# Optimization experiments

Measured on AMD Instinct MI355X. Metric: run time of the kernel, lower is better.

Reference implementation:

```python
import jax, jax.numpy as jnp
import numpy as np
import math

N_HIDDEN = 256
N_BLOCKS = 15
N_BINARY = 8
NODE_DIM = 16
EDGE_DIM = 4
N_NODES = 20000
N_EDGES = 100000


def setup_inputs() -> dict:
    key = jax.random.key(0)
    ks = iter(jax.random.split(key, 64))

    def lin(i, o):
        return (jax.random.normal(next(ks), (i, o), jnp.float32) / np.sqrt(i)).astype(jnp.float32)

    def lin_s(i, o):  # stacked over N_BLOCKS layers
        return (jax.random.normal(next(ks), (N_BLOCKS, i, o), jnp.float32) / np.sqrt(i)).astype(jnp.float32)

    inp = {
        "x": jax.random.uniform(next(ks), (N_NODES, NODE_DIM), jnp.float32),
        "edge_index": jax.random.randint(next(ks), (2, N_EDGES), 0, N_NODES, jnp.int32),
        "edge_attr": jax.random.uniform(next(ks), (N_EDGES, EDGE_DIM), jnp.float32),
        # conv1: in = NODE_DIM
        "Wq1": lin(NODE_DIM, N_HIDDEN), "bq1": jnp.zeros((N_HIDDEN,), jnp.float32),
        "Wk1": lin(NODE_DIM, N_HIDDEN), "bk1": jnp.zeros((N_HIDDEN,), jnp.float32),
        "Wv1": lin(NODE_DIM, N_HIDDEN), "bv1": jnp.zeros((N_HIDDEN,), jnp.float32),
        "We1": lin(EDGE_DIM, N_HIDDEN),  # lin_edge has no bias in PyG TransformerConv
        "Ws1": lin(NODE_DIM, N_HIDDEN), "bs1": jnp.zeros((N_HIDDEN,), jnp.float32),
        # 15 residual blocks: in = N_HIDDEN, stacked params
        "Wq": lin_s(N_HIDDEN, N_HIDDEN), "bq": jnp.zeros((N_BLOCKS, N_HIDDEN), jnp.float32),
        "Wk": lin_s(N_HIDDEN, N_HIDDEN), "bk": jnp.zeros((N_BLOCKS, N_HIDDEN), jnp.float32),
        "Wv": lin_s(N_HIDDEN, N_HIDDEN), "bv": jnp.zeros((N_BLOCKS, N_HIDDEN), jnp.float32),
        "We": lin_s(EDGE_DIM, N_HIDDEN),
        "Ws": lin_s(N_HIDDEN, N_HIDDEN), "bs": jnp.zeros((N_BLOCKS, N_HIDDEN), jnp.float32),
        # output head
        "Wl": lin(N_HIDDEN, N_BINARY), "bl": jnp.zeros((N_BINARY,), jnp.float32),
        "scale": jnp.asarray([2.0 ** i for i in range(N_BINARY)], jnp.float32),
    }
    return inp


def _tconv(h, ea_emb_src_params, src, dst, n):
    """PyG TransformerConv (heads=1) with edge features."""
    wq, bq, wk, bk, wv, bv, we, ws, bs, ea = ea_emb_src_params
    q = h @ wq + bq          # [N, C]
    k = h @ wk + bk
    v = h @ wv + bv
    e = ea @ we              # [E, C] edge embedding
    ke = k[src] + e          # [E, C]
    alpha = jnp.sum(q[dst] * ke, axis=-1) / math.sqrt(N_HIDDEN)  # [E]
    m = jax.ops.segment_max(alpha, dst, num_segments=n)
    a = jnp.exp(alpha - m[dst])
    s = jax.ops.segment_sum(a, dst, num_segments=n)
    attn = a / (s[dst] + 1e-16)
    out = jax.ops.segment_sum(attn[:, None] * (v[src] + e), dst, num_segments=n)
    return out + h @ ws + bs  # root_weight skip


def reference(x, edge_index, edge_attr,
              Wq1, bq1, Wk1, bk1, Wv1, bv1, We1, Ws1, bs1,
              Wq, bq, Wk, bk, Wv, bv, We, Ws, bs,
              Wl, bl, scale):
    n = x.shape[0]
    src, dst = edge_index[0], edge_index[1]
    h = jnp.log(x + 1.0)
    ea = jnp.log(edge_attr + 1.0)
    h = _tconv(h, (Wq1, bq1, Wk1, bk1, Wv1, bv1, We1, Ws1, bs1, ea), src, dst, n)

    def block(carry, p):
        wq, bq_, wk, bk_, wv, bv_, we, ws, bs_ = p
        std = jax.lax.stop_gradient(jnp.std(carry, axis=-1, ddof=1, keepdims=True))
        h2 = jax.nn.relu(carry / std)
        y = _tconv(h2, (wq, bq_, wk, bk_, wv, bv_, we, ws, bs_, ea), src, dst, n)
        return carry + y, None

    h, _ = jax.lax.scan(block, h, (Wq, bq, Wk, bk, Wv, bv, We, Ws, bs))
    h = h / math.sqrt(N_BLOCKS)
    h = h @ Wl + bl
    return jnp.sum(h * scale, axis=-1, keepdims=True)
```

## Files before the change

### kernel.cpp

```cpp
#include <hip/hip_runtime.h>
#include <math.h>

typedef short bf16x8 __attribute__((ext_vector_type(8)));
typedef float f32x4 __attribute__((ext_vector_type(4)));
typedef _Float16 h16x8 __attribute__((ext_vector_type(8)));
typedef _Float16 h16x4 __attribute__((ext_vector_type(4)));
typedef _Float16 h16x2 __attribute__((ext_vector_type(2)));

static __device__ __forceinline__ float wred_sum(float v){
  #pragma unroll
  for (int o = 32; o > 0; o >>= 1) v += __shfl_xor(v, o, 64);
  return v;
}

static __device__ __forceinline__ unsigned short f2bf(float x){
  union { float f; unsigned int u; } c; c.f = x;
  unsigned int u = c.u;
  return (unsigned short)((u + 0x7FFFu + ((u >> 16) & 1u)) >> 16);
}

__global__ void prep_kernel(const float* __restrict__ x, const float* __restrict__ ea_in,
                            float* __restrict__ hx, float* __restrict__ ea,
                            int nx, int ne){
  int i = blockIdx.x * 256 + threadIdx.x;
  if (i < nx) hx[i] = logf(x[i] + 1.f);
  if (i < ne) ea[i] = logf(ea_in[i] + 1.f);
}

__global__ void zero_kernel(int* __restrict__ c, int n){
  int i = blockIdx.x * 256 + threadIdx.x;
  if (i < n) c[i] = 0;
}

__global__ void hist_kernel(const int* __restrict__ dst, int* __restrict__ counts, int E){
  int i = blockIdx.x * 256 + threadIdx.x;
  if (i < E) atomicAdd(&counts[dst[i]], 1);
}

__global__ __launch_bounds__(1024) void scan_kernel(const int* __restrict__ counts,
                                                    int* __restrict__ row_ptr,
                                                    int* __restrict__ cursor, int N){
  __shared__ int sh[1024];
  __shared__ int carry_s;
  int t = threadIdx.x;
  if (t == 0) carry_s = 0;
  __syncthreads();
  for (int base = 0; base < N; base += 1024){
    int i = base + t;
    int v = (i < N) ? counts[i] : 0;
    sh[t] = v;
    __syncthreads();
    for (int o = 1; o < 1024; o <<= 1){
      int add = (t >= o) ? sh[t - o] : 0;
      __syncthreads();
      sh[t] += add;
      __syncthreads();
    }
    int incl = sh[t];
    int carry = carry_s;
    if (i < N){ int ex = carry + incl - v; row_ptr[i] = ex; cursor[i] = ex; }
    __syncthreads();
    if (t == 1023) carry_s = carry + incl;
    __syncthreads();
  }
  if (t == 0) row_ptr[N] = carry_s;
}

__global__ void scatter_kernel(const int* __restrict__ src, const int* __restrict__ dst,
                               const float* __restrict__ ea,
                               int* __restrict__ cursor,
                               int* __restrict__ src_csr, float* __restrict__ ea_csr, int E){
  int i = blockIdx.x * 256 + threadIdx.x;
  if (i < E){
    int p = atomicAdd(&cursor[dst[i]], 1);
    src_csr[p] = src[i];
    *(float4*)&ea_csr[(size_t)p * 4] = *(const float4*)&ea[(size_t)i * 4];
  }
}

__global__ void wlscale_kernel(const float* __restrict__ Wl, const float* __restrict__ bl,
                               const float* __restrict__ scale, float* __restrict__ wlsc){
  int c = threadIdx.x;
  float s = 0.f;
  #pragma unroll
  for (int j = 0; j < 8; j++) s += Wl[c * 8 + j] * scale[j];
  wlsc[c] = s;
  if (c == 0){
    float b = 0.f;
    #pragma unroll
    for (int j = 0; j < 8; j++) b += bl[j] * scale[j];
    wlsc[256] = b;
  }
}

__global__ __launch_bounds__(256) void pack_w_kernel(
    const float* __restrict__ Wq, const float* __restrict__ Wk,
    const float* __restrict__ Wv, const float* __restrict__ Ws,
    unsigned short* __restrict__ Wp)
{
  __shared__ float t[32][33];
  int l   = blockIdx.z;
  int k0  = blockIdx.x * 32;
  int n0g = blockIdx.y * 32;
  int w   = n0g >> 8;
  int n0  = n0g & 255;
  const float* W = ((w == 0) ? Wq : (w == 1) ? Wk : (w == 2) ? Wv : Ws) + (size_t)l * 65536;
  int rr = threadIdx.x >> 3;
  int cc = (threadIdx.x & 7) * 4;
  float4 vv = *(const float4*)&W[(size_t)(k0 + rr) * 256 + n0 + cc];
  t[rr][cc + 0] = vv.x; t[rr][cc + 1] = vv.y; t[rr][cc + 2] = vv.z; t[rr][cc + 3] = vv.w;
  __syncthreads();
  ushort4 o;
  o.x = f2bf(t[cc + 0][rr]);
  o.y = f2bf(t[cc + 1][rr]);
  o.z = f2bf(t[cc + 2][rr]);
  o.w = f2bf(t[cc + 3][rr]);
  *(ushort4*)&Wp[(size_t)l * 262144 + (size_t)(n0g + rr) * 256 + k0 + cc] = o;
}

__global__ void pack_b_kernel(const float* __restrict__ bq, const float* __restrict__ bk,
                              const float* __restrict__ bv, const float* __restrict__ bs,
                              float* __restrict__ bp){
  int i = blockIdx.x * 256 + threadIdx.x;
  if (i < 15 * 256){
    int l = i >> 8, n = i & 255;
    bp[l * 1024 + 0   + n] = bq[i];
    bp[l * 1024 + 256 + n] = bk[i];
    bp[l * 1024 + 512 + n] = bv[i];
    bp[l * 1024 + 768 + n] = bs[i];
  }
}

__global__ __launch_bounds__(256) void pack_wqe_kernel(
    const float* __restrict__ Wq, const float* __restrict__ We,
    const float* __restrict__ bq, float* __restrict__ Wqe, float* __restrict__ bqe)
{
  __shared__ float We_s[1024];
  int l = blockIdx.x;
  for (int i = threadIdx.x; i < 1024; i += 256) We_s[i] = We[(size_t)l * 1024 + i];
  __syncthreads();
  int k = threadIdx.x;
  const float* wrow = Wq + (size_t)l * 65536 + (size_t)k * 256;
  float s0 = 0.f, s1 = 0.f, s2 = 0.f, s3 = 0.f;
  for (int c = 0; c < 256; c++){
    float wv = wrow[c];
    s0 += wv * We_s[c];
    s1 += wv * We_s[256 + c];
    s2 += wv * We_s[512 + c];
    s3 += wv * We_s[768 + c];
  }
  float4 o; o.x = s0; o.y = s1; o.z = s2; o.w = s3;
  *(float4*)&Wqe[((size_t)l * 256 + k) * 4] = o;
  if (k < 4){
    float b = 0.f;
    for (int c = 0; c < 256; c++) b += bq[l * 256 + c] * We_s[k * 256 + c];
    bqe[l * 4 + k] = b;
  }
}

__global__ __launch_bounds__(256) void qwe1_kernel(const _Float16* __restrict__ qkvh,
                                                   const float* __restrict__ We1,
                                                   float* __restrict__ qwe, int N){
  __shared__ float We_s[1024];
  for (int i = threadIdx.x; i < 1024; i += 256) We_s[i] = We1[i];
  __syncthreads();
  int wid = threadIdx.x >> 6, lane = threadIdx.x & 63;
  int n = blockIdx.x * 4 + wid;
  if (n >= N) return;
  int c0 = lane * 4;
  h16x4 qr = *(const h16x4*)&qkvh[(size_t)n * 768 + c0];
  float q0 = (float)qr[0], q1 = (float)qr[1], q2 = (float)qr[2], q3 = (float)qr[3];
  float4 o;
  #pragma unroll
  for (int j = 0; j < 4; j++){
    float s = q0 * We_s[j * 256 + c0] + q1 * We_s[j * 256 + c0 + 1]
            + q2 * We_s[j * 256 + c0 + 2] + q3 * We_s[j * 256 + c0 + 3];
    s = wred_sum(s);
    if (j == 0) o.x = s; else if (j == 1) o.y = s; else if (j == 2) o.z = s; else o.w = s;
  }
  if (lane == 0) *(float4*)&qwe[(size_t)n * 4] = o;
}

__global__ __launch_bounds__(256) void gemm1_kernel(
    const float* __restrict__ A,
    const float* __restrict__ W0, const float* __restrict__ W1,
    const float* __restrict__ W2, const float* __restrict__ W3,
    const float* __restrict__ B0, const float* __restrict__ B1,
    const float* __restrict__ B2, const float* __restrict__ B3,
    _Float16* __restrict__ qkvh, _Float16* __restrict__ slh, int N)
{
  __shared__ float As[64][16];
  int nb = blockIdx.x * 64;
  {
    int row = nb + (threadIdx.x >> 2);
    int qq = (threadIdx.x & 3) * 4;
    float4 a = make_float4(0.f, 0.f, 0.f, 0.f);
    if (row < N) a = *(const float4*)&A[row * 16 + qq];
    *(float4*)&As[threadIdx.x >> 2][qq] = a;
  }
  __syncthreads();
  int col = threadIdx.x;
  #pragma unroll
  for (int w = 0; w < 4; w++){
    const float* W  = (w == 0) ? W0 : (w == 1) ? W1 : (w == 2) ? W2 : W3;
    const float* Bi = (w == 0) ? B0 : (w == 1) ? B1 : (w == 2) ? B2 : B3;
    float wr[16];
    #pragma unroll
    for (int kk = 0; kk < 16; kk++) wr[kk] = W[kk * 256 + col];
    float bias = Bi[col];
    for (int r = 0; r < 64; r++){
      int row = nb + r;
      if (row >= N) break;
      float acc = bias;
      #pragma unroll
      for (int kk = 0; kk < 16; kk++) acc += As[r][kk] * wr[kk];
      if (w < 3) qkvh[(size_t)row * 768 + w * 256 + col] = (_Float16)acc;
      else       slh[(size_t)row * 256 + col] = (_Float16)acc;
    }
  }
}

__global__ __launch_bounds__(256, 2) void gemm_mfma_kernel(
    const unsigned short* __restrict__ A,
    const unsigned short* __restrict__ Wp,
    const float* __restrict__ bp,
    _Float16* __restrict__ qkvh,
    _Float16* __restrict__ slh,
    int M)
{
  __shared__ unsigned short lds[2 * 128 * 64];
  unsigned short* ldsA = lds;
  unsigned short* ldsB = lds + 128 * 64;
  const int tid  = threadIdx.x;
  const int wave = tid >> 6, lane = tid & 63;
  const int wm = wave >> 1, wn = wave & 1;
  const int m0 = blockIdx.x * 128;
  const int n0 = blockIdx.y * 128;

  f32x4 acc[4][4] = {};

  const int srow  = lane >> 3;
  const int sc16  = lane & 7;
  const int skgrp = sc16 ^ (srow & 7);

  for (int k0 = 0; k0 < 256; k0 += 64){
    #pragma unroll
    for (int it = 0; it < 4; ++it){
      int lrow = wave * 32 + it * 8;
      const unsigned short* gA = A + (size_t)(m0 + lrow + srow) * 256 + k0 + skgrp * 8;
      __builtin_amdgcn_global_load_lds((const __attribute__((address_space(1))) unsigned int*)gA,
          (__attribute__((address_space(3))) unsigned int*)(ldsA + lrow * 64), 16, 0, 0);
      const unsigned short* gB = Wp + (size_t)(n0 + lrow + srow) * 256 + k0 + skgrp * 8;
      __builtin_amdgcn_global_load_lds((const __attribute__((address_space(1))) unsigned int*)gB,
          (__attribute__((address_space(3))) unsigned int*)(ldsB + lrow * 64), 16, 0, 0);
    }
    __syncthreads();

    bf16x8 af[4][2], bfr[4][2];
    #pragma unroll
    for (int mb = 0; mb < 4; ++mb){
      int r = wm * 64 + mb * 16 + (lane & 15);
      #pragma unroll
      for (int ks = 0; ks < 2; ++ks){
        int kg = ks * 4 + (lane >> 4);
        af[mb][ks] = *(const bf16x8*)&ldsA[r * 64 + ((kg ^ (r & 7)) * 8)];
      }
    }
    #pragma unroll
    for (int nb = 0; nb < 4; ++nb){
      int r = wn * 64 + nb * 16 + (lane & 15);
      #pragma unroll
      for (int ks = 0; ks < 2; ++ks){
        int kg = ks * 4 + (lane >> 4);
        bfr[nb][ks] = *(const bf16x8*)&ldsB[r * 64 + ((kg ^ (r & 7)) * 8)];
      }
    }
    #pragma unroll
    for (int mb = 0; mb < 4; ++mb){
      #pragma unroll
      for (int nb = 0; nb < 4; ++nb){
        acc[mb][nb] = __builtin_amdgcn_mfma_f32_16x16x32_bf16(af[mb][0], bfr[nb][0], acc[mb][nb], 0, 0, 0);
        acc[mb][nb] = __builtin_amdgcn_mfma_f32_16x16x32_bf16(af[mb][1], bfr[nb][1], acc[mb][nb], 0, 0, 0);
      }
    }
    __syncthreads();
  }

  #pragma unroll
  for (int nb = 0; nb < 4; ++nb){
    int col = n0 + wn * 64 + nb * 16 + (lane & 15);
    float bias = bp[col];
    #pragma unroll
    for (int mb = 0; mb < 4; ++mb){
      #pragma unroll
      for (int r4 = 0; r4 < 4; ++r4){
        int row = m0 + wm * 64 + mb * 16 + (lane >> 4) * 4 + r4;
        if (row < M){
          float o = acc[mb][nb][r4] + bias;
          if (col < 768) qkvh[(size_t)row * 768 + col] = (_Float16)o;
          else           slh[(size_t)row * 256 + (col - 768)] = (_Float16)o;
        }
      }
    }
  }
}

__global__ __launch_bounds__(256) void agg_kernel(
    const _Float16* __restrict__ qkvh,
    const _Float16* __restrict__ slh,
    const float* __restrict__ qwe,
    const float* __restrict__ ea_csr,
    const int* __restrict__ src_csr,
    const float* __restrict__ We,
    const float* __restrict__ Wqe_next,
    const float* __restrict__ bqe_next,
    const int* __restrict__ row_ptr,
    const float* __restrict__ h_in, float* __restrict__ h_out,
    unsigned short* __restrict__ h2b, float* __restrict__ qwe_out,
    int RESID, int N)
{
  int wid = threadIdx.x >> 6, lane = threadIdx.x & 63;
  int n = blockIdx.x * 4 + wid;
  if (n >= N) return;
  int c0 = lane * 4;
  int glane = lane >> 4;
  int slane = lane & 15;

  float4 qwe4 = *(const float4*)&qwe[(size_t)n * 4];
  const _Float16* qrow = qkvh + (size_t)n * 768 + slane * 16;
  union { h16x8 v; h16x2 p[4]; } qa, qb;
  qa.v = *(const h16x8*)qrow;
  qb.v = *(const h16x8*)(qrow + 8);

  float m = -INFINITY, ssum = 0.f;
  float a0 = 0.f, a1 = 0.f, a2 = 0.f, a3 = 0.f;
  float ec0 = 0.f, ec1 = 0.f, ec2 = 0.f, ec3 = 0.f;
  int e0 = row_ptr[n], e1 = row_ptr[n + 1];

  for (int base = e0; base < e1; base += 4){
    int cnt = min(4, e1 - base);
    int eg = base + ((glane < cnt) ? glane : (cnt - 1));
    int sg = src_csr[eg];
    float4 eag = *(const float4*)&ea_csr[(size_t)eg * 4];
    const _Float16* krow = qkvh + (size_t)sg * 768 + 256 + slane * 16;
    union { h16x8 v; h16x2 p[4]; } ka, kb;
    ka.v = *(const h16x8*)krow;
    kb.v = *(const h16x8*)(krow + 8);
    float dot = 0.f;
    #pragma unroll
    for (int u = 0; u < 4; ++u){
#if __has_builtin(__builtin_amdgcn_fdot2)
      dot = __builtin_amdgcn_fdot2(qa.p[u], ka.p[u], dot, false);
      dot = __builtin_amdgcn_fdot2(qb.p[u], kb.p[u], dot, false);
#else
      dot += (float)qa.p[u][0] * (float)ka.p[u][0] + (float)qa.p[u][1] * (float)ka.p[u][1];
      dot += (float)qb.p[u][0] * (float)kb.p[u][0] + (float)qb.p[u][1] * (float)kb.p[u][1];
#endif
    }
    #pragma unroll
    for (int o = 1; o < 16; o <<= 1) dot += __shfl_xor(dot, o, 64);
    float alpha_g = (dot + qwe4.x * eag.x + qwe4.y * eag.y + qwe4.z * eag.z + qwe4.w * eag.w) * 0.0625f;
    float aj[4];
    #pragma unroll
    for (int j = 0; j < 4; ++j){
      aj[j] = __shfl(alpha_g, j << 4, 64);
      if (j >= cnt) aj[j] = -INFINITY;
    }
    float mc = fmaxf(fmaxf(aj[0], aj[1]), fmaxf(aj[2], aj[3]));
    float mn = fmaxf(m, mc);
    float corr = expf(m - mn);
    float w0 = (0 < cnt) ? expf(aj[0] - mn) : 0.f;
    float w1 = (1 < cnt) ? expf(aj[1] - mn) : 0.f;
    float w2 = (2 < cnt) ? expf(aj[2] - mn) : 0.f;
    float w3 = (3 < cnt) ? expf(aj[3] - mn) : 0.f;
    ssum = ssum * corr + (w0 + w1 + w2 + w3);
    a0 *= corr; a1 *= corr; a2 *= corr; a3 *= corr;
    ec0 *= corr; ec1 *= corr; ec2 *= corr; ec3 *= corr;
    m = mn;
    float wj[4] = {w0, w1, w2, w3};
    #pragma unroll
    for (int j = 0; j < 4; ++j){
      if (j < cnt){
        int sj = __shfl(sg, j << 4, 64);
        h16x4 vr = *(const h16x4*)&qkvh[(size_t)sj * 768 + 512 + c0];
        float4 er = *(const float4*)&ea_csr[(size_t)(base + j) * 4];
        a0 += wj[j] * (float)vr[0];
        a1 += wj[j] * (float)vr[1];
        a2 += wj[j] * (float)vr[2];
        a3 += wj[j] * (float)vr[3];
        ec0 += wj[j] * er.x;
        ec1 += wj[j] * er.y;
        ec2 += wj[j] * er.z;
        ec3 += wj[j] * er.w;
      }
    }
  }

  float inv = 1.f / (ssum + 1e-16f);
  float4 W0 = *(const float4*)&We[0 * 256 + c0];
  float4 W1 = *(const float4*)&We[1 * 256 + c0];
  float4 W2 = *(const float4*)&We[2 * 256 + c0];
  float4 W3 = *(const float4*)&We[3 * 256 + c0];
  float emb0 = ec0 * W0.x + ec1 * W1.x + ec2 * W2.x + ec3 * W3.x;
  float emb1 = ec0 * W0.y + ec1 * W1.y + ec2 * W2.y + ec3 * W3.y;
  float emb2 = ec0 * W0.z + ec1 * W1.z + ec2 * W2.z + ec3 * W3.z;
  float emb3 = ec0 * W0.w + ec1 * W1.w + ec2 * W2.w + ec3 * W3.w;
  h16x4 slv4 = *(const h16x4*)&slh[(size_t)n * 256 + c0];
  float y0 = (a0 + emb0) * inv + (float)slv4[0];
  float y1 = (a1 + emb1) * inv + (float)slv4[1];
  float y2 = (a2 + emb2) * inv + (float)slv4[2];
  float y3 = (a3 + emb3) * inv + (float)slv4[3];
  float o0, o1, o2, o3;
  if (RESID){
    float4 hp = *(const float4*)&h_in[(size_t)n * 256 + c0];
    o0 = hp.x + y0; o1 = hp.y + y1; o2 = hp.z + y2; o3 = hp.w + y3;
  } else {
    o0 = y0; o1 = y1; o2 = y2; o3 = y3;
  }
  float4 ho; ho.x = o0; ho.y = o1; ho.z = o2; ho.w = o3;
  *(float4*)&h_out[(size_t)n * 256 + c0] = ho;
  float mean = wred_sum(o0 + o1 + o2 + o3) * (1.f / 256.f);
  float d0 = o0 - mean, d1 = o1 - mean, d2 = o2 - mean, d3 = o3 - mean;
  float var = wred_sum(d0 * d0 + d1 * d1 + d2 * d2 + d3 * d3) * (1.f / 255.f);
  float invstd = 1.f / sqrtf(var);
  float t0 = fmaxf(o0 * invstd, 0.f);
  float t1 = fmaxf(o1 * invstd, 0.f);
  float t2 = fmaxf(o2 * invstd, 0.f);
  float t3 = fmaxf(o3 * invstd, 0.f);
  ushort4 hb;
  hb.x = f2bf(t0); hb.y = f2bf(t1); hb.z = f2bf(t2); hb.w = f2bf(t3);
  *(ushort4*)&h2b[(size_t)n * 256 + c0] = hb;
  if (Wqe_next){
    float4 g0 = *(const float4*)&Wqe_next[(c0 + 0) * 4];
    float4 g1 = *(const float4*)&Wqe_next[(c0 + 1) * 4];
    float4 g2 = *(const float4*)&Wqe_next[(c0 + 2) * 4];
    float4 g3 = *(const float4*)&Wqe_next[(c0 + 3) * 4];
    float s0 = t0 * g0.x + t1 * g1.x + t2 * g2.x + t3 * g3.x;
    float s1 = t0 * g0.y + t1 * g1.y + t2 * g2.y + t3 * g3.y;
    float s2 = t0 * g0.z + t1 * g1.z + t2 * g2.z + t3 * g3.z;
    float s3 = t0 * g0.w + t1 * g1.w + t2 * g2.w + t3 * g3.w;
    s0 = wred_sum(s0); s1 = wred_sum(s1); s2 = wred_sum(s2); s3 = wred_sum(s3);
    if (lane == 0){
      float4 bq4 = *(const float4*)bqe_next;
      float4 o; o.x = s0 + bq4.x; o.y = s1 + bq4.y; o.z = s2 + bq4.z; o.w = s3 + bq4.w;
      *(float4*)&qwe_out[(size_t)n * 4] = o;
    }
  }
}

__global__ __launch_bounds__(256) void head_kernel(const float* __restrict__ h,
                                                   const float* __restrict__ wlsc,
                                                   float* __restrict__ out, int N){
  int wid = threadIdx.x >> 6, lane = threadIdx.x & 63;
  int n = blockIdx.x * 4 + wid;
  if (n >= N) return;
  int c0 = lane * 4;
  float4 hv = *(const float4*)&h[(size_t)n * 256 + c0];
  float4 wv = *(const float4*)&wlsc[c0];
  float p = hv.x * wv.x + hv.y * wv.y + hv.z * wv.z + hv.w * wv.w;
  p = wred_sum(p);
  if (lane == 0) out[n] = p * (1.f / sqrtf(15.f)) + wlsc[256];
}

extern "C" void kernel_launch(void* const* d_in, const int* in_sizes, int n_in,
                              void* d_out, int out_size, void* d_ws, size_t ws_size,
                              hipStream_t stream)
{
  const float* x     = (const float*)d_in[0];
  const int*   eidx  = (const int*)d_in[1];
  const float* Wq1 = (const float*)d_in[3];  const float* bq1 = (const float*)d_in[4];
  const float* Wk1 = (const float*)d_in[5];  const float* bk1 = (const float*)d_in[6];
  const float* Wv1 = (const float*)d_in[7];  const float* bv1 = (const float*)d_in[8];
  const float* We1 = (const float*)d_in[9];
  const float* Ws1 = (const float*)d_in[10]; const float* bs1 = (const float*)d_in[11];
  const float* Wq = (const float*)d_in[12];  const float* bq = (const float*)d_in[13];
  const float* Wk = (const float*)d_in[14];  const float* bk = (const float*)d_in[15];
  const float* Wv = (const float*)d_in[16];  const float* bv = (const float*)d_in[17];
  const float* We = (const float*)d_in[18];
  const float* Ws = (const float*)d_in[19];  const float* bs = (const float*)d_in[20];
  const float* Wl = (const float*)d_in[21];  const float* bl = (const float*)d_in[22];
  const float* scale = (const float*)d_in[23];
  (void)n_in; (void)ws_size;

  int N = in_sizes[0] / 16;
  int E = in_sizes[2] / 4;
  int Mpad = (N + 127) & ~127;
  float* out = (float*)d_out;
  (void)out_size;

  char* p = (char*)d_ws;
  auto alloc = [&](size_t bytes) -> char* {
    char* r = p; p += (bytes + 255) & ~(size_t)255; return r;
  };
  float* hx   = (float*)alloc((size_t)N * 16 * 4);
  float* ea   = (float*)alloc((size_t)E * 4 * 4);
  float* h    = (float*)alloc((size_t)N * 256 * 4);
  unsigned short* h2b = (unsigned short*)alloc((size_t)Mpad * 256 * 2);
  _Float16* qkvh = (_Float16*)alloc((size_t)N * 768 * 2);
  _Float16* slh  = (_Float16*)alloc((size_t)N * 256 * 2);
  float* qwe  = (float*)alloc((size_t)N * 4 * 4);
  float* ea_csr = (float*)alloc((size_t)E * 4 * 4);
  int* src_csr  = (int*)alloc((size_t)E * 4);
  unsigned short* Wp  = (unsigned short*)alloc((size_t)15 * 1024 * 256 * 2);
  float* bp   = (float*)alloc((size_t)15 * 1024 * 4);
  float* Wqe  = (float*)alloc((size_t)15 * 256 * 4 * 4);
  float* bqe  = (float*)alloc((size_t)15 * 4 * 4);
  float* wlsc = (float*)alloc(257 * 4);
  int* counts  = (int*)alloc((size_t)N * 4);
  int* cursor  = (int*)alloc((size_t)N * 4);
  int* row_ptr = (int*)alloc(((size_t)N + 1) * 4);

  const int* srcp = eidx;
  const int* dstp = eidx + E;

  int nx = N * 16, ne = E * 4;
  int big = nx > ne ? nx : ne;

  zero_kernel<<<(N + 255) / 256, 256, 0, stream>>>(counts, N);
  prep_kernel<<<(big + 255) / 256, 256, 0, stream>>>(x, (const float*)d_in[2], hx, ea, nx, ne);
  hist_kernel<<<(E + 255) / 256, 256, 0, stream>>>(dstp, counts, E);
  scan_kernel<<<1, 1024, 0, stream>>>(counts, row_ptr, cursor, N);
  scatter_kernel<<<(E + 255) / 256, 256, 0, stream>>>(srcp, dstp, ea, cursor,
                                                      src_csr, ea_csr, E);
  wlscale_kernel<<<1, 256, 0, stream>>>(Wl, bl, scale, wlsc);
  pack_w_kernel<<<dim3(8, 32, 15), 256, 0, stream>>>(Wq, Wk, Wv, Ws, Wp);
  pack_b_kernel<<<15, 256, 0, stream>>>(bq, bk, bv, bs, bp);
  pack_wqe_kernel<<<15, 256, 0, stream>>>(Wq, We, bq, Wqe, bqe);

  gemm1_kernel<<<(N + 63) / 64, 256, 0, stream>>>(hx, Wq1, Wk1, Wv1, Ws1,
                                                  bq1, bk1, bv1, bs1, qkvh, slh, N);
  qwe1_kernel<<<(N + 3) / 4, 256, 0, stream>>>(qkvh, We1, qwe, N);
  agg_kernel<<<(N + 3) / 4, 256, 0, stream>>>(qkvh, slh, qwe, ea_csr, src_csr, We1,
                                              Wqe, bqe, row_ptr,
                                              h, h, h2b, qwe, 0, N);

  for (int l = 0; l < 15; l++){
    gemm_mfma_kernel<<<dim3(Mpad / 128, 8), 256, 0, stream>>>(
        h2b, Wp + (size_t)l * 262144, bp + (size_t)l * 1024, qkvh, slh, N);
    const float* wqe_n = (l < 14) ? (Wqe + (size_t)(l + 1) * 1024) : nullptr;
    const float* bqe_n = (l < 14) ? (bqe + (size_t)(l + 1) * 4) : nullptr;
    agg_kernel<<<(N + 3) / 4, 256, 0, stream>>>(qkvh, slh, qwe, ea_csr, src_csr,
                                                We + (size_t)l * 1024,
                                                wqe_n, bqe_n, row_ptr,
                                                h, h, h2b, qwe, 1, N);
  }

  head_kernel<<<(N + 3) / 4, 256, 0, stream>>>(h, wlsc, out, N);
}
```

Measured before the change: 1.256 ms.

## Widen edge batches in aggregation, fuse head, swizzle GEMM tiles, warp-scan CSR

The aggregation kernel now handles 8 edges per step instead of 4, with 8 lanes per edge, which halves the online-softmax iterations for a given degree. The output head is folded into the last aggregation launch, so the final h store and the separate head kernel go away. The GEMM remaps block indices so consecutive blocks walk the N tiles of one M tile, for better L2 reuse, and raises its occupancy hint to 3. The scan kernel replaces its LDS Hillis-Steele loop with wavefront shuffle scans, removing many barriers.

```diff
diff --git a/kernel.cpp b/kernel.cpp
--- a/kernel.cpp
+++ b/kernel.cpp
@@ -40,27 +40,37 @@
 __global__ __launch_bounds__(1024) void scan_kernel(const int* __restrict__ counts,
                                                     int* __restrict__ row_ptr,
                                                     int* __restrict__ cursor, int N){
-  __shared__ int sh[1024];
+  __shared__ int woff[16];
   __shared__ int carry_s;
-  int t = threadIdx.x;
+  int t = threadIdx.x, lane = t & 63, wid = t >> 6;
   if (t == 0) carry_s = 0;
   __syncthreads();
   for (int base = 0; base < N; base += 1024){
     int i = base + t;
     int v = (i < N) ? counts[i] : 0;
-    sh[t] = v;
+    int incl = v;
+    #pragma unroll
+    for (int o = 1; o < 64; o <<= 1){
+      int tmp = __shfl_up(incl, o, 64);
+      if (lane >= o) incl += tmp;
+    }
+    if (lane == 63) woff[wid] = incl;
     __syncthreads();
-    for (int o = 1; o < 1024; o <<= 1){
-      int add = (t >= o) ? sh[t - o] : 0;
-      __syncthreads();
-      sh[t] += add;
-      __syncthreads();
-    }
-    int incl = sh[t];
-    int carry = carry_s;
-    if (i < N){ int ex = carry + incl - v; row_ptr[i] = ex; cursor[i] = ex; }
+    if (t < 16){
+      int w = woff[t];
+      int inc2 = w;
+      #pragma unroll
+      for (int o = 1; o < 16; o <<= 1){
+        int tmp = __shfl_up(inc2, o, 16);
+        if (t >= o) inc2 += tmp;
+      }
+      woff[t] = inc2 - w;
+    }
     __syncthreads();
-    if (t == 1023) carry_s = carry + incl;
+    int ex = carry_s + woff[wid] + incl - v;
+    if (i < N){ row_ptr[i] = ex; cursor[i] = ex; }
+    __syncthreads();
+    if (t == 1023) carry_s = ex + v;
     __syncthreads();
   }
   if (t == 0) row_ptr[N] = carry_s;
@@ -220,7 +230,7 @@
   }
 }
 
-__global__ __launch_bounds__(256, 2) void gemm_mfma_kernel(
+__global__ __launch_bounds__(256, 3) void gemm_mfma_kernel(
     const unsigned short* __restrict__ A,
     const unsigned short* __restrict__ Wp,
     const float* __restrict__ bp,
@@ -234,8 +244,11 @@
   const int tid  = threadIdx.x;
   const int wave = tid >> 6, lane = tid & 63;
   const int wm = wave >> 1, wn = wave & 1;
-  const int m0 = blockIdx.x * 128;
-  const int n0 = blockIdx.y * 128;
+  const int rt  = (int)gridDim.x;
+  const int lin = (int)blockIdx.x + rt * (int)blockIdx.y;
+  const int gt  = (lin & 7) * rt + (lin >> 3);
+  const int m0 = (gt >> 3) * 128;
+  const int n0 = (gt & 7) * 128;
 
   f32x4 acc[4][4] = {};
 
@@ -317,71 +330,76 @@
     const int* __restrict__ row_ptr,
     const float* __restrict__ h_in, float* __restrict__ h_out,
     unsigned short* __restrict__ h2b, float* __restrict__ qwe_out,
-    int RESID, int N)
+    const float* __restrict__ wlsc, float* __restrict__ out,
+    int RESID, int LAST, int N)
 {
   int wid = threadIdx.x >> 6, lane = threadIdx.x & 63;
   int n = blockIdx.x * 4 + wid;
   if (n >= N) return;
   int c0 = lane * 4;
-  int glane = lane >> 4;
-  int slane = lane & 15;
+  int glane = lane >> 3;
+  int slane = lane & 7;
 
   float4 qwe4 = *(const float4*)&qwe[(size_t)n * 4];
-  const _Float16* qrow = qkvh + (size_t)n * 768 + slane * 16;
-  union { h16x8 v; h16x2 p[4]; } qa, qb;
-  qa.v = *(const h16x8*)qrow;
-  qb.v = *(const h16x8*)(qrow + 8);
+  const _Float16* qrow = qkvh + (size_t)n * 768 + slane * 32;
+  union hu { h16x8 v; h16x2 p[4]; };
+  hu qf[4];
+  #pragma unroll
+  for (int u = 0; u < 4; ++u) qf[u].v = *(const h16x8*)(qrow + u * 8);
 
   float m = -INFINITY, ssum = 0.f;
   float a0 = 0.f, a1 = 0.f, a2 = 0.f, a3 = 0.f;
   float ec0 = 0.f, ec1 = 0.f, ec2 = 0.f, ec3 = 0.f;
   int e0 = row_ptr[n], e1 = row_ptr[n + 1];
 
-  for (int base = e0; base < e1; base += 4){
-    int cnt = min(4, e1 - base);
+  for (int base = e0; base < e1; base += 8){
+    int cnt = min(8, e1 - base);
     int eg = base + ((glane < cnt) ? glane : (cnt - 1));
     int sg = src_csr[eg];
     float4 eag = *(const float4*)&ea_csr[(size_t)eg * 4];
-    const _Float16* krow = qkvh + (size_t)sg * 768 + 256 + slane * 16;
-    union { h16x8 v; h16x2 p[4]; } ka, kb;
-    ka.v = *(const h16x8*)krow;
-    kb.v = *(const h16x8*)(krow + 8);
+    const _Float16* krow = qkvh + (size_t)sg * 768 + 256 + slane * 32;
     float dot = 0.f;
     #pragma unroll
     for (int u = 0; u < 4; ++u){
+      hu kf;
+      kf.v = *(const h16x8*)(krow + u * 8);
+      #pragma unroll
+      for (int pp = 0; pp < 4; ++pp){
 #if __has_builtin(__builtin_amdgcn_fdot2)
-      dot = __builtin_amdgcn_fdot2(qa.p[u], ka.p[u], dot, false);
-      dot = __builtin_amdgcn_fdot2(qb.p[u], kb.p[u], dot, false);
+        dot = __builtin_amdgcn_fdot2(qf[u].p[pp], kf.p[pp], dot, false);
 #else
-      dot += (float)qa.p[u][0] * (float)ka.p[u][0] + (float)qa.p[u][1] * (float)ka.p[u][1];
-      dot += (float)qb.p[u][0] * (float)kb.p[u][0] + (float)qb.p[u][1] * (float)kb.p[u][1];
+        dot += (float)qf[u].p[pp][0] * (float)kf.p[pp][0] + (float)qf[u].p[pp][1] * (float)kf.p[pp][1];
 #endif
-    }
-    #pragma unroll
-    for (int o = 1; o < 16; o <<= 1) dot += __shfl_xor(dot, o, 64);
+      }
+    }
+    #pragma unroll
+    for (int o = 1; o < 8; o <<= 1) dot += __shfl_xor(dot, o, 64);
     float alpha_g = (dot + qwe4.x * eag.x + qwe4.y * eag.y + qwe4.z * eag.z + qwe4.w * eag.w) * 0.0625f;
-    float aj[4];
-    #pragma unroll
-    for (int j = 0; j < 4; ++j){
-      aj[j] = __shfl(alpha_g, j << 4, 64);
+    float aj[8];
+    #pragma unroll
+    for (int j = 0; j < 8; ++j){
+      aj[j] = __shfl(alpha_g, j << 3, 64);
       if (j >= cnt) aj[j] = -INFINITY;
     }
-    float mc = fmaxf(fmaxf(aj[0], aj[1]), fmaxf(aj[2], aj[3]));
+    float mc = fmaxf(fmaxf(fmaxf(aj[0], aj[1]), fmaxf(aj[2], aj[3])),
+                     fmaxf(fmaxf(aj[4], aj[5]), fmaxf(aj[6], aj[7])));
     float mn = fmaxf(m, mc);
     float corr = expf(m - mn);
-    float w0 = (0 < cnt) ? expf(aj[0] - mn) : 0.f;
-    float w1 = (1 < cnt) ? expf(aj[1] - mn) : 0.f;
-    float w2 = (2 < cnt) ? expf(aj[2] - mn) : 0.f;
-    float w3 = (3 < cnt) ? expf(aj[3] - mn) : 0.f;
-    ssum = ssum * corr + (w0 + w1 + w2 + w3);
+    float wj[8];
+    float wtot = 0.f;
+    #pragma unroll
+    for (int j = 0; j < 8; ++j){
+      wj[j] = (j < cnt) ? expf(aj[j] - mn) : 0.f;
+      wtot += wj[j];
+    }
+    ssum = ssum * corr + wtot;
     a0 *= corr; a1 *= corr; a2 *= corr; a3 *= corr;
     ec0 *= corr; ec1 *= corr; ec2 *= corr; ec3 *= corr;
     m = mn;
-    float wj[4] = {w0, w1, w2, w3};
-    #pragma unroll
-    for (int j = 0; j < 4; ++j){
+    #pragma unroll
+    for (int j = 0; j < 8; ++j){
       if (j < cnt){
-        int sj = __shfl(sg, j << 4, 64);
+        int sj = __shfl(sg, j << 3, 64);
         h16x4 vr = *(const h16x4*)&qkvh[(size_t)sj * 768 + 512 + c0];
         float4 er = *(const float4*)&ea_csr[(size_t)(base + j) * 4];
         a0 += wj[j] * (float)vr[0];
@@ -416,6 +434,13 @@
     o0 = hp.x + y0; o1 = hp.y + y1; o2 = hp.z + y2; o3 = hp.w + y3;
   } else {
     o0 = y0; o1 = y1; o2 = y2; o3 = y3;
+  }
+  if (LAST){
+    float4 wv = *(const float4*)&wlsc[c0];
+    float pp = o0 * wv.x + o1 * wv.y + o2 * wv.z + o3 * wv.w;
+    pp = wred_sum(pp);
+    if (lane == 0) out[n] = pp * (1.f / sqrtf(15.f)) + wlsc[256];
+    return;
   }
   float4 ho; ho.x = o0; ho.y = o1; ho.z = o2; ho.w = o3;
   *(float4*)&h_out[(size_t)n * 256 + c0] = ho;
@@ -448,20 +473,6 @@
   }
 }
 
-__global__ __launch_bounds__(256) void head_kernel(const float* __restrict__ h,
-                                                   const float* __restrict__ wlsc,
-                                                   float* __restrict__ out, int N){
-  int wid = threadIdx.x >> 6, lane = threadIdx.x & 63;
-  int n = blockIdx.x * 4 + wid;
-  if (n >= N) return;
-  int c0 = lane * 4;
-  float4 hv = *(const float4*)&h[(size_t)n * 256 + c0];
-  float4 wv = *(const float4*)&wlsc[c0];
-  float p = hv.x * wv.x + hv.y * wv.y + hv.z * wv.z + hv.w * wv.w;
-  p = wred_sum(p);
-  if (lane == 0) out[n] = p * (1.f / sqrtf(15.f)) + wlsc[256];
-}
-
 extern "C" void kernel_launch(void* const* d_in, const int* in_sizes, int n_in,
                               void* d_out, int out_size, void* d_ws, size_t ws_size,
                               hipStream_t stream)
@@ -532,18 +543,17 @@
   qwe1_kernel<<<(N + 3) / 4, 256, 0, stream>>>(qkvh, We1, qwe, N);
   agg_kernel<<<(N + 3) / 4, 256, 0, stream>>>(qkvh, slh, qwe, ea_csr, src_csr, We1,
                                               Wqe, bqe, row_ptr,
-                                              h, h, h2b, qwe, 0, N);
+                                              h, h, h2b, qwe, wlsc, out, 0, 0, N);
 
   for (int l = 0; l < 15; l++){
     gemm_mfma_kernel<<<dim3(Mpad / 128, 8), 256, 0, stream>>>(
         h2b, Wp + (size_t)l * 262144, bp + (size_t)l * 1024, qkvh, slh, N);
+    int last = (l == 14);
     const float* wqe_n = (l < 14) ? (Wqe + (size_t)(l + 1) * 1024) : nullptr;
     const float* bqe_n = (l < 14) ? (bqe + (size_t)(l + 1) * 4) : nullptr;
     agg_kernel<<<(N + 3) / 4, 256, 0, stream>>>(qkvh, slh, qwe, ea_csr, src_csr,
                                                 We + (size_t)l * 1024,
                                                 wqe_n, bqe_n, row_ptr,
-                                                h, h, h2b, qwe, 1, N);
-  }
-
-  head_kernel<<<(N + 3) / 4, 256, 0, stream>>>(h, wlsc, out, N);
-}
+                                                h, h, h2b, qwe, wlsc, out, 1, last, N);
+  }
+}
```

New measurement: 1.259 ms. No clear change (+0.2%).
